# Kernel optimization log

Hardware: AMD Instinct MI355X
Metric: run time of the kernel (lower is better)

## Reference

```python
import jax, jax.numpy as jnp
import numpy as np

N = 50000
E = 800000
F_IN, F_HID, F_OUT = 128, 256, 128


def setup_inputs() -> dict:
    key = jax.random.key(0)
    ks = jax.random.split(key, 8)
    x = jax.random.normal(ks[0], (N, F_IN), dtype=jnp.float32)
    edge_index = jax.random.randint(ks[1], (2, E), 0, N, dtype=jnp.int64)
    # SAGEConv params: lin_l acts on aggregated neighbors (has bias), lin_r on root.
    def w(k, fi, fo):
        return jax.random.normal(k, (fi, fo), dtype=jnp.float32) / np.sqrt(fi)
    return {
        "x": x,
        "edge_index": edge_index,
        "W1_l": w(ks[2], F_IN, F_HID),
        "W1_r": w(ks[3], F_IN, F_HID),
        "b1": jnp.zeros((F_HID,), dtype=jnp.float32),
        "W2_l": w(ks[4], F_HID, F_OUT),
        "W2_r": w(ks[5], F_HID, F_OUT),
        "b2": jnp.zeros((F_OUT,), dtype=jnp.float32),
    }


def _sage_conv(x, src, dst, W_l, W_r, b):
    # mean aggregation of source features onto destination nodes
    msg_sum = jax.ops.segment_sum(x[src], dst, num_segments=N)   # [N, F]
    deg = jax.ops.segment_sum(jnp.ones((src.shape[0],), x.dtype), dst,
                              num_segments=N)                    # [N]
    mean = msg_sum / jnp.maximum(deg, 1.0)[:, None]
    return mean @ W_l + x @ W_r + b


def reference(x, edge_index, W1_l, W1_r, b1, W2_l, W2_r, b2):
    src, dst = edge_index[0], edge_index[1]
    h = jax.nn.relu(_sage_conv(x, src, dst, W1_l, W1_r, b1))
    # dropout is identity in eval mode (p=0.0)
    out = _sage_conv(h, src, dst, W2_l, W2_r, b2)
    return out
```

## Files before the change

### kernel.cpp

```cpp
#include <hip/hip_runtime.h>

constexpr int NN = 50000;
constexpr int EE = 800000;
constexpr int FI = 128;
constexpr int FO = 128;

typedef __attribute__((ext_vector_type(4))) float f32x4;
typedef __attribute__((ext_vector_type(8))) short bf16x8;

__device__ inline unsigned short f2bf(float f) {
    union { float f; unsigned u; } v; v.f = f;
    unsigned r = v.u + 0x7FFFu + ((v.u >> 16) & 1u);
    return (unsigned short)(r >> 16);
}
__device__ inline float bf2f(unsigned short u) {
    union { unsigned u; float f; } v; v.u = ((unsigned)u) << 16; return v.f;
}


__global__ void deg_i_kernel(const int* __restrict__ ei, int* __restrict__ deg) {
    int e = blockIdx.x * blockDim.x + threadIdx.x;
    if (e < EE) atomicAdd(&deg[ei[EE + e]], 1);
}

__global__ void rdeg_i_kernel(const int* __restrict__ deg, float* __restrict__ rdeg) {
    int n = blockIdx.x * blockDim.x + threadIdx.x;
    if (n < NN) rdeg[n] = 1.0f / fmaxf((float)deg[n], 1.0f);
}

constexpr int SCAN_NBLK = (NN + 1023) / 1024;

__global__ __launch_bounds__(1024) void scan_phase1(const int* __restrict__ deg,
                                                    int* __restrict__ rowptr,
                                                    int* __restrict__ bsum) {
    __shared__ int wsum[16];
    const int tid = threadIdx.x;
    const int lane = tid & 63;
    const int wid = tid >> 6;
    int i = blockIdx.x * 1024 + tid;
    int v = (i < NN) ? deg[i] : 0;
    int s = v;
#pragma unroll
    for (int off = 1; off < 64; off <<= 1) {
        int t = __shfl_up(s, off, 64);
        if (lane >= off) s += t;
    }
    if (lane == 63) wsum[wid] = s;
    __syncthreads();
    if (wid == 0) {
        int ws = (lane < 16) ? wsum[lane] : 0;
#pragma unroll
        for (int off = 1; off < 16; off <<= 1) {
            int t = __shfl_up(ws, off, 64);
            if (lane >= off) ws += t;
        }
        if (lane < 16) wsum[lane] = ws;
    }
    __syncthreads();
    int woff = (wid > 0) ? wsum[wid - 1] : 0;
    if (i < NN) rowptr[i] = woff + s - v;
    if (tid == 0) bsum[blockIdx.x] = wsum[15];
}

__global__ void scan_phase2(int* __restrict__ bsum) {
    int lane = threadIdx.x;
    int v = (lane < SCAN_NBLK) ? bsum[lane] : 0;
    int s = v;
#pragma unroll
    for (int off = 1; off < 64; off <<= 1) {
        int t = __shfl_up(s, off, 64);
        if (lane >= off) s += t;
    }
    if (lane < SCAN_NBLK) bsum[lane] = s - v;
}

__global__ void scan_phase3(int* __restrict__ rowptr, const int* __restrict__ bsum) {
    int i = blockIdx.x * blockDim.x + threadIdx.x;
    if (i < NN) rowptr[i] += bsum[i >> 10];
}

__global__ void slot_kernel(const int* __restrict__ ei, int* __restrict__ rowptr,
                            int* __restrict__ csr_src) {
    int e = blockIdx.x * blockDim.x + threadIdx.x;
    if (e < EE) {
        int src = ei[e];
        int dst = ei[EE + e];
        int slot = atomicAdd(&rowptr[dst], 1);
        csr_src[slot] = src;
    }
}


__global__ __launch_bounds__(256) void gather_mean_bf16(
    const int* __restrict__ rowptr, const int* __restrict__ csr_src,
    const float* __restrict__ rdeg,
    unsigned short* __restrict__ A1)
{
    int node = blockIdx.x * 4 + (threadIdx.x >> 6);
    if (node >= NN) return;
    int lane = threadIdx.x & 63;
    int f = lane * 2;
    int start = (node == 0) ? 0 : rowptr[node - 1];
    int end = rowptr[node];
    float ax0 = 0.f, ay0 = 0.f, ax1 = 0.f, ay1 = 0.f;
    int j = start;
    for (; j + 1 < end; j += 2) {
        int s0 = csr_src[j];
        int s1 = csr_src[j + 1];
        ushort2 v0 = *reinterpret_cast<const ushort2*>(A1 + (size_t)s0 * 256 + 128 + f);
        ushort2 v1 = *reinterpret_cast<const ushort2*>(A1 + (size_t)s1 * 256 + 128 + f);
        ax0 += bf2f(v0.x); ay0 += bf2f(v0.y);
        ax1 += bf2f(v1.x); ay1 += bf2f(v1.y);
    }
    if (j < end) {
        int s0 = csr_src[j];
        ushort2 v0 = *reinterpret_cast<const ushort2*>(A1 + (size_t)s0 * 256 + 128 + f);
        ax0 += bf2f(v0.x); ay0 += bf2f(v0.y);
    }
    float s = rdeg[node];
    ushort2 o;
    o.x = f2bf((ax0 + ax1) * s);
    o.y = f2bf((ay0 + ay1) * s);
    *reinterpret_cast<ushort2*>(A1 + (size_t)node * 256 + f) = o;
}

__global__ __launch_bounds__(256) void gather_accum_f32(
    const int* __restrict__ rowptr, const int* __restrict__ csr_src,
    const float* __restrict__ rdeg, const unsigned short* __restrict__ g2b,
    float* __restrict__ outp)
{
    int node = blockIdx.x * 4 + (threadIdx.x >> 6);
    if (node >= NN) return;
    int lane = threadIdx.x & 63;
    int f = lane * 2;
    int start = (node == 0) ? 0 : rowptr[node - 1];
    int end = rowptr[node];
    float ax0 = 0.f, ay0 = 0.f, ax1 = 0.f, ay1 = 0.f;
    int j = start;
    for (; j + 1 < end; j += 2) {
        int s0 = csr_src[j];
        int s1 = csr_src[j + 1];
        ushort2 v0 = *reinterpret_cast<const ushort2*>(g2b + (size_t)s0 * 128 + f);
        ushort2 v1 = *reinterpret_cast<const ushort2*>(g2b + (size_t)s1 * 128 + f);
        ax0 += bf2f(v0.x); ay0 += bf2f(v0.y);
        ax1 += bf2f(v1.x); ay1 += bf2f(v1.y);
    }
    if (j < end) {
        int s0 = csr_src[j];
        ushort2 v0 = *reinterpret_cast<const ushort2*>(g2b + (size_t)s0 * 128 + f);
        ax0 += bf2f(v0.x); ay0 += bf2f(v0.y);
    }
    float s = rdeg[node];
    float* p = outp + (size_t)node * FO + f;
    float2 o = *reinterpret_cast<float2*>(p);
    o.x += (ax0 + ax1) * s;
    o.y += (ay0 + ay1) * s;
    *reinterpret_cast<float2*>(p) = o;
}


__global__ void cast_x_kernel(const float* __restrict__ x,
                              unsigned short* __restrict__ A1) {
    int i = blockIdx.x * blockDim.x + threadIdx.x;
    if (i >= NN * 32) return;
    int n = i >> 5;
    int c4 = (i & 31) * 4;
    float4 v = *reinterpret_cast<const float4*>(x + (size_t)n * FI + c4);
    ushort4 o;
    o.x = f2bf(v.x); o.y = f2bf(v.y); o.z = f2bf(v.z); o.w = f2bf(v.w);
    *reinterpret_cast<ushort4*>(A1 + (size_t)n * 256 + 128 + c4) = o;
}

__global__ void prep_weights(const float* __restrict__ W1l, const float* __restrict__ W1r,
                             const float* __restrict__ W2l, const float* __restrict__ W2r,
                             unsigned short* __restrict__ B1T,
                             unsigned short* __restrict__ B2T) {
    int i = blockIdx.x * blockDim.x + threadIdx.x;
    if (i >= 256 * 256) return;
    int n = i >> 8, k = i & 255;
    float v1 = (k < 128) ? W1l[(size_t)k * 256 + n] : W1r[(size_t)(k - 128) * 256 + n];
    B1T[(size_t)n * 256 + k] = f2bf(v1);
    float v2 = (n < 128) ? W2r[(size_t)k * 128 + n] : W2l[(size_t)k * 128 + (n - 128)];
    B2T[(size_t)n * 256 + k] = f2bf(v2);
}

constexpr int GPAD = 80;

template<int MODE>
__global__ __launch_bounds__(256) void mfma_gemm(
    const unsigned short* __restrict__ A,
    const unsigned short* __restrict__ BT,
    const float* __restrict__ bias,
    unsigned short* __restrict__ out_bf,
    float* __restrict__ out_f0,
    unsigned short* __restrict__ g2b)
{
    __shared__ unsigned short Al[64][GPAD];
    __shared__ unsigned short Bl[256][GPAD];

    const int t = threadIdx.x;
    const int wid = t >> 6;
    const int lane = t & 63;
    const int l15 = lane & 15;
    const int lhi = lane >> 4;
    const int row0 = blockIdx.x * 64;

    f32x4 acc[16];
#pragma unroll
    for (int n = 0; n < 16; ++n) acc[n] = f32x4{0.f, 0.f, 0.f, 0.f};

    for (int kc = 0; kc < 256; kc += 64) {
        __syncthreads();
#pragma unroll
        for (int i = 0; i < 2; ++i) {
            int idx = t + i * 256;
            int r = idx >> 3;
            int c = (idx & 7) * 8;
            int rr = row0 + r;
            if (rr >= NN) rr = NN - 1;
            *reinterpret_cast<uint4*>(&Al[r][c]) =
                *reinterpret_cast<const uint4*>(A + (size_t)rr * 256 + kc + c);
        }
#pragma unroll
        for (int i = 0; i < 8; ++i) {
            int idx = t + i * 256;
            int r = idx >> 3;
            int c = (idx & 7) * 8;
            *reinterpret_cast<uint4*>(&Bl[r][c]) =
                *reinterpret_cast<const uint4*>(BT + (size_t)r * 256 + kc + c);
        }
        __syncthreads();
#pragma unroll
        for (int ks = 0; ks < 64; ks += 32) {
            bf16x8 a = *reinterpret_cast<const bf16x8*>(&Al[wid * 16 + l15][ks + lhi * 8]);
#pragma unroll
            for (int n = 0; n < 16; ++n) {
                bf16x8 b = *reinterpret_cast<const bf16x8*>(&Bl[n * 16 + l15][ks + lhi * 8]);
                acc[n] = __builtin_amdgcn_mfma_f32_16x16x32_bf16(a, b, acc[n], 0, 0, 0);
            }
        }
    }

#pragma unroll
    for (int n = 0; n < 16; ++n) {
        int col = n * 16 + l15;
#pragma unroll
        for (int j = 0; j < 4; ++j) {
            int row = row0 + wid * 16 + lhi * 4 + j;
            if (row < NN) {
                float v = acc[n][j];
                if (MODE == 0) {
                    v += bias[col];
                    v = fmaxf(v, 0.f);
                    out_bf[(size_t)row * 256 + col] = f2bf(v);
                } else {
                    if (col < 128) out_f0[(size_t)row * 128 + col] = v + bias[col];
                    else           g2b[(size_t)row * 128 + (col - 128)] = f2bf(v);
                }
            }
        }
    }
}


extern "C" void kernel_launch(void* const* d_in, const int* in_sizes, int n_in,
                              void* d_out, int out_size, void* d_ws, size_t ws_size,
                              hipStream_t stream) {
    const float* x   = (const float*)d_in[0];
    const int*   ei  = (const int*)d_in[1];
    const float* W1l = (const float*)d_in[2];
    const float* W1r = (const float*)d_in[3];
    const float* b1  = (const float*)d_in[4];
    const float* W2l = (const float*)d_in[5];
    const float* W2r = (const float*)d_in[6];
    const float* b2  = (const float*)d_in[7];
    float*       out = (float*)d_out;

    const size_t needed =
        ((size_t)NN * 3 + EE + (size_t)NN * 128 * 2 + 65536 + 64) * 4;
    if (ws_size < needed) return;

    int*            deg_i   = (int*)d_ws;
    int*            rowptr  = deg_i + NN;
    int*            csr_src = rowptr + NN;
    float*          rdeg    = (float*)(csr_src + EE);
    unsigned short* A1      = (unsigned short*)(rdeg + NN);
    unsigned short* g2b     = A1;
    unsigned short* h       = A1 + (size_t)NN * 256;
    unsigned short* B1T     = h + (size_t)NN * 256;
    unsigned short* B2T     = B1T + 256 * 256;
    int*            bsum    = (int*)(B2T + 256 * 256);

    hipMemsetAsync(deg_i, 0, (size_t)NN * sizeof(int), stream);
    prep_weights<<<256, 256, 0, stream>>>(W1l, W1r, W2l, W2r, B1T, B2T);
    cast_x_kernel<<<(NN * 32 + 255) / 256, 256, 0, stream>>>(x, A1);
    deg_i_kernel<<<(EE + 255) / 256, 256, 0, stream>>>(ei, deg_i);
    scan_phase1<<<SCAN_NBLK, 1024, 0, stream>>>(deg_i, rowptr, bsum);
    scan_phase2<<<1, 64, 0, stream>>>(bsum);
    scan_phase3<<<(NN + 255) / 256, 256, 0, stream>>>(rowptr, bsum);
    rdeg_i_kernel<<<(NN + 255) / 256, 256, 0, stream>>>(deg_i, rdeg);
    slot_kernel<<<(EE + 255) / 256, 256, 0, stream>>>(ei, rowptr, csr_src);

    gather_mean_bf16<<<(NN + 3) / 4, 256, 0, stream>>>(rowptr, csr_src, rdeg, A1);
    mfma_gemm<0><<<(NN + 63) / 64, 256, 0, stream>>>(A1, B1T, b1, h, nullptr, nullptr);

    mfma_gemm<1><<<(NN + 63) / 64, 256, 0, stream>>>(h, B2T, b2, nullptr, out, g2b);

    gather_accum_f32<<<(NN + 3) / 4, 256, 0, stream>>>(rowptr, csr_src, rdeg, g2b, out);
}
```

Measured before the change: 388.5 us.

## Fuse rdeg into scan, unroll gathers by four, retile GEMM waves 2x2

Computes the reciprocal degree inside the first scan phase, which removes one kernel launch. Both gather kernels now unroll by four with independent accumulators so more loads are in flight per wave. The MFMA GEMM splits its waves into a 2x2 grid with 32 rows by 128 columns each, so every B fragment loaded from LDS feeds two MFMAs. The LDS padding also changes from 80 to 72, which alters the bank-conflict pattern.

After: 348.1 us. -10.4%, faster.

```diff
diff --git a/kernel.cpp b/kernel.cpp
--- a/kernel.cpp
+++ b/kernel.cpp
@@ -23,22 +23,19 @@
     if (e < EE) atomicAdd(&deg[ei[EE + e]], 1);
 }
 
-__global__ void rdeg_i_kernel(const int* __restrict__ deg, float* __restrict__ rdeg) {
-    int n = blockIdx.x * blockDim.x + threadIdx.x;
-    if (n < NN) rdeg[n] = 1.0f / fmaxf((float)deg[n], 1.0f);
-}
-
 constexpr int SCAN_NBLK = (NN + 1023) / 1024;
 
 __global__ __launch_bounds__(1024) void scan_phase1(const int* __restrict__ deg,
                                                     int* __restrict__ rowptr,
-                                                    int* __restrict__ bsum) {
+                                                    int* __restrict__ bsum,
+                                                    float* __restrict__ rdeg) {
     __shared__ int wsum[16];
     const int tid = threadIdx.x;
     const int lane = tid & 63;
     const int wid = tid >> 6;
     int i = blockIdx.x * 1024 + tid;
     int v = (i < NN) ? deg[i] : 0;
+    if (i < NN) rdeg[i] = 1.0f / fmaxf((float)v, 1.0f);
     int s = v;
 #pragma unroll
     for (int off = 1; off < 64; off <<= 1) {
@@ -103,24 +100,31 @@
     int start = (node == 0) ? 0 : rowptr[node - 1];
     int end = rowptr[node];
     float ax0 = 0.f, ay0 = 0.f, ax1 = 0.f, ay1 = 0.f;
+    float ax2 = 0.f, ay2 = 0.f, ax3 = 0.f, ay3 = 0.f;
     int j = start;
-    for (; j + 1 < end; j += 2) {
+    for (; j + 3 < end; j += 4) {
         int s0 = csr_src[j];
         int s1 = csr_src[j + 1];
+        int s2 = csr_src[j + 2];
+        int s3 = csr_src[j + 3];
         ushort2 v0 = *reinterpret_cast<const ushort2*>(A1 + (size_t)s0 * 256 + 128 + f);
         ushort2 v1 = *reinterpret_cast<const ushort2*>(A1 + (size_t)s1 * 256 + 128 + f);
+        ushort2 v2 = *reinterpret_cast<const ushort2*>(A1 + (size_t)s2 * 256 + 128 + f);
+        ushort2 v3 = *reinterpret_cast<const ushort2*>(A1 + (size_t)s3 * 256 + 128 + f);
         ax0 += bf2f(v0.x); ay0 += bf2f(v0.y);
         ax1 += bf2f(v1.x); ay1 += bf2f(v1.y);
-    }
-    if (j < end) {
+        ax2 += bf2f(v2.x); ay2 += bf2f(v2.y);
+        ax3 += bf2f(v3.x); ay3 += bf2f(v3.y);
+    }
+    for (; j < end; ++j) {
         int s0 = csr_src[j];
         ushort2 v0 = *reinterpret_cast<const ushort2*>(A1 + (size_t)s0 * 256 + 128 + f);
         ax0 += bf2f(v0.x); ay0 += bf2f(v0.y);
     }
     float s = rdeg[node];
     ushort2 o;
-    o.x = f2bf((ax0 + ax1) * s);
-    o.y = f2bf((ay0 + ay1) * s);
+    o.x = f2bf(((ax0 + ax1) + (ax2 + ax3)) * s);
+    o.y = f2bf(((ay0 + ay1) + (ay2 + ay3)) * s);
     *reinterpret_cast<ushort2*>(A1 + (size_t)node * 256 + f) = o;
 }
 
@@ -136,16 +140,23 @@
     int start = (node == 0) ? 0 : rowptr[node - 1];
     int end = rowptr[node];
     float ax0 = 0.f, ay0 = 0.f, ax1 = 0.f, ay1 = 0.f;
+    float ax2 = 0.f, ay2 = 0.f, ax3 = 0.f, ay3 = 0.f;
     int j = start;
-    for (; j + 1 < end; j += 2) {
+    for (; j + 3 < end; j += 4) {
         int s0 = csr_src[j];
         int s1 = csr_src[j + 1];
+        int s2 = csr_src[j + 2];
+        int s3 = csr_src[j + 3];
         ushort2 v0 = *reinterpret_cast<const ushort2*>(g2b + (size_t)s0 * 128 + f);
         ushort2 v1 = *reinterpret_cast<const ushort2*>(g2b + (size_t)s1 * 128 + f);
+        ushort2 v2 = *reinterpret_cast<const ushort2*>(g2b + (size_t)s2 * 128 + f);
+        ushort2 v3 = *reinterpret_cast<const ushort2*>(g2b + (size_t)s3 * 128 + f);
         ax0 += bf2f(v0.x); ay0 += bf2f(v0.y);
         ax1 += bf2f(v1.x); ay1 += bf2f(v1.y);
-    }
-    if (j < end) {
+        ax2 += bf2f(v2.x); ay2 += bf2f(v2.y);
+        ax3 += bf2f(v3.x); ay3 += bf2f(v3.y);
+    }
+    for (; j < end; ++j) {
         int s0 = csr_src[j];
         ushort2 v0 = *reinterpret_cast<const ushort2*>(g2b + (size_t)s0 * 128 + f);
         ax0 += bf2f(v0.x); ay0 += bf2f(v0.y);
@@ -153,8 +164,8 @@
     float s = rdeg[node];
     float* p = outp + (size_t)node * FO + f;
     float2 o = *reinterpret_cast<float2*>(p);
-    o.x += (ax0 + ax1) * s;
-    o.y += (ay0 + ay1) * s;
+    o.x += ((ax0 + ax1) + (ax2 + ax3)) * s;
+    o.y += ((ay0 + ay1) + (ay2 + ay3)) * s;
     *reinterpret_cast<float2*>(p) = o;
 }
 
@@ -184,7 +195,7 @@
     B2T[(size_t)n * 256 + k] = f2bf(v2);
 }
 
-constexpr int GPAD = 80;
+constexpr int GPAD = 72;
 
 template<int MODE>
 __global__ __launch_bounds__(256) void mfma_gemm(
@@ -200,14 +211,18 @@
 
     const int t = threadIdx.x;
     const int wid = t >> 6;
+    const int wr = wid >> 1;
+    const int wc = wid & 1;
     const int lane = t & 63;
     const int l15 = lane & 15;
     const int lhi = lane >> 4;
     const int row0 = blockIdx.x * 64;
 
-    f32x4 acc[16];
-#pragma unroll
-    for (int n = 0; n < 16; ++n) acc[n] = f32x4{0.f, 0.f, 0.f, 0.f};
+    f32x4 acc[2][8];
+#pragma unroll
+    for (int m = 0; m < 2; ++m)
+#pragma unroll
+        for (int n = 0; n < 8; ++n) acc[m][n] = f32x4{0.f, 0.f, 0.f, 0.f};
 
     for (int kc = 0; kc < 256; kc += 64) {
         __syncthreads();
@@ -232,30 +247,36 @@
         __syncthreads();
 #pragma unroll
         for (int ks = 0; ks < 64; ks += 32) {
-            bf16x8 a = *reinterpret_cast<const bf16x8*>(&Al[wid * 16 + l15][ks + lhi * 8]);
-#pragma unroll
-            for (int n = 0; n < 16; ++n) {
-                bf16x8 b = *reinterpret_cast<const bf16x8*>(&Bl[n * 16 + l15][ks + lhi * 8]);
-                acc[n] = __builtin_amdgcn_mfma_f32_16x16x32_bf16(a, b, acc[n], 0, 0, 0);
+            bf16x8 a0 = *reinterpret_cast<const bf16x8*>(&Al[wr * 32 + l15][ks + lhi * 8]);
+            bf16x8 a1 = *reinterpret_cast<const bf16x8*>(&Al[wr * 32 + 16 + l15][ks + lhi * 8]);
+#pragma unroll
+            for (int n = 0; n < 8; ++n) {
+                bf16x8 b = *reinterpret_cast<const bf16x8*>(
+                    &Bl[wc * 128 + n * 16 + l15][ks + lhi * 8]);
+                acc[0][n] = __builtin_amdgcn_mfma_f32_16x16x32_bf16(a0, b, acc[0][n], 0, 0, 0);
+                acc[1][n] = __builtin_amdgcn_mfma_f32_16x16x32_bf16(a1, b, acc[1][n], 0, 0, 0);
             }
         }
     }
 
 #pragma unroll
-    for (int n = 0; n < 16; ++n) {
-        int col = n * 16 + l15;
-#pragma unroll
-        for (int j = 0; j < 4; ++j) {
-            int row = row0 + wid * 16 + lhi * 4 + j;
-            if (row < NN) {
-                float v = acc[n][j];
-                if (MODE == 0) {
-                    v += bias[col];
-                    v = fmaxf(v, 0.f);
-                    out_bf[(size_t)row * 256 + col] = f2bf(v);
-                } else {
-                    if (col < 128) out_f0[(size_t)row * 128 + col] = v + bias[col];
-                    else           g2b[(size_t)row * 128 + (col - 128)] = f2bf(v);
+    for (int n = 0; n < 8; ++n) {
+        int col = wc * 128 + n * 16 + l15;
+#pragma unroll
+        for (int m = 0; m < 2; ++m) {
+#pragma unroll
+            for (int j = 0; j < 4; ++j) {
+                int row = row0 + wr * 32 + m * 16 + lhi * 4 + j;
+                if (row < NN) {
+                    float v = acc[m][n][j];
+                    if (MODE == 0) {
+                        v += bias[col];
+                        v = fmaxf(v, 0.f);
+                        out_bf[(size_t)row * 256 + col] = f2bf(v);
+                    } else {
+                        if (col < 128) out_f0[(size_t)row * 128 + col] = v + bias[col];
+                        else           g2b[(size_t)row * 128 + (col - 128)] = f2bf(v);
+                    }
                 }
             }
         }
@@ -295,10 +316,9 @@
     prep_weights<<<256, 256, 0, stream>>>(W1l, W1r, W2l, W2r, B1T, B2T);
     cast_x_kernel<<<(NN * 32 + 255) / 256, 256, 0, stream>>>(x, A1);
     deg_i_kernel<<<(EE + 255) / 256, 256, 0, stream>>>(ei, deg_i);
-    scan_phase1<<<SCAN_NBLK, 1024, 0, stream>>>(deg_i, rowptr, bsum);
+    scan_phase1<<<SCAN_NBLK, 1024, 0, stream>>>(deg_i, rowptr, bsum, rdeg);
     scan_phase2<<<1, 64, 0, stream>>>(bsum);
     scan_phase3<<<(NN + 255) / 256, 256, 0, stream>>>(rowptr, bsum);
-    rdeg_i_kernel<<<(NN + 255) / 256, 256, 0, stream>>>(deg_i, rdeg);
     slot_kernel<<<(EE + 255) / 256, 256, 0, stream>>>(ei, rowptr, csr_src);
 
     gather_mean_bf16<<<(NN + 3) / 4, 256, 0, stream>>>(rowptr, csr_src, rdeg, A1);
```
